# Optimization experiments

Hardware: AMD Instinct MI355X
Metric: run time of the kernel (lower is better)

Reference implementation:

```python
import jax, jax.numpy as jnp
import numpy as np

DIM = 768
HEADS = 12
HEAD_DIM = DIM // HEADS
WS = 32                      # window_size (Wh == Ww)
N = WS * WS + 1              # tokens = patches + CLS
B = 8
NUM_REL = (2 * WS - 1) * (2 * WS - 1) + 3


def _rel_pos_index():
    # Mirrors the torch buffer construction (meshgrid indexing='ij').
    coords = np.stack(np.meshgrid(np.arange(WS), np.arange(WS), indexing='ij')).reshape(2, -1)
    rel = (coords[:, :, None] - coords[:, None, :]).transpose(1, 2, 0)  # [M, M, 2]
    rel[..., 0] += WS - 1
    rel[..., 1] += WS - 1
    rel[..., 0] *= 2 * WS - 1
    idx = np.zeros((N, N), dtype=np.int32)
    idx[1:, 1:] = rel.sum(-1)
    idx[0, :] = NUM_REL - 3
    idx[:, 0] = NUM_REL - 2
    idx[0, 0] = NUM_REL - 1
    return idx


def setup_inputs() -> dict:
    key = jax.random.key(0)
    ks = jax.random.split(key, 4)
    s = DIM ** -0.5
    return {
        "x": jax.random.normal(ks[0], (B, N, DIM), dtype=jnp.float32),
        "qkv_w": jax.random.normal(ks[1], (3 * DIM, DIM), dtype=jnp.float32) * s,
        "q_bias": jnp.zeros((DIM,), dtype=jnp.float32),
        "v_bias": jnp.zeros((DIM,), dtype=jnp.float32),
        "rpb_table": jax.random.normal(ks[2], (NUM_REL, HEADS), dtype=jnp.float32) * 0.02,
        "proj_w": jax.random.normal(ks[3], (DIM, DIM), dtype=jnp.float32) * s,
        "proj_b": jnp.zeros((DIM,), dtype=jnp.float32),
        "rel_pos_index": jnp.asarray(_rel_pos_index()),
    }


def reference(x, qkv_w, q_bias, v_bias, rpb_table, proj_w, proj_b, rel_pos_index):
    Bx, Nx, C = x.shape
    scale = HEAD_DIM ** -0.5
    # qkv bias = [q_bias, zeros, v_bias] (k has no bias)
    qkv_bias = jnp.concatenate([q_bias, jnp.zeros_like(v_bias), v_bias])
    qkv = x @ qkv_w.T + qkv_bias                           # [B, N, 3*C]
    qkv = qkv.reshape(Bx, Nx, 3, HEADS, HEAD_DIM).transpose(2, 0, 3, 1, 4)
    q, k, v = qkv[0] * scale, qkv[1], qkv[2]               # [B, H, N, d]
    attn = jnp.einsum('bhqd,bhkd->bhqk', q, k)             # [B, H, N, N]
    rpb = rpb_table[rel_pos_index]                         # [N, N, H] gather
    attn = attn + rpb.transpose(2, 0, 1)[None]             # broadcast over batch
    attn = jax.nn.softmax(attn, axis=-1)
    out = jnp.einsum('bhqk,bhkd->bhqd', attn, v)           # [B, H, N, d]
    out = out.transpose(0, 2, 1, 3).reshape(Bx, Nx, -1)    # [B, N, C]
    return out @ proj_w.T + proj_b
```

## Files before the change

kernel.cpp:

```cpp
#include <hip/hip_runtime.h>

typedef _Float16 f16;
typedef __attribute__((ext_vector_type(8))) _Float16 f16x8;
typedef __attribute__((ext_vector_type(4))) float f32x4;

#define BATCH 8
#define NTOK 1025
#define DIM 768
#define HEADS 12
#define HD 64
#define MTOT (BATCH * NTOK)
#define MPAD 8320
#define NQP 1088
#define NKP 1088
#define KTILES 17
#define NUMREL 3972

__device__ __forceinline__ int imin(int a, int b) { return a < b ? a : b; }

__device__ __forceinline__ void gl_lds16(const f16* g, f16* l) {
  __builtin_amdgcn_global_load_lds(
      (const __attribute__((address_space(1))) unsigned int*)g,
      (__attribute__((address_space(3))) unsigned int*)l, 16, 0, 0);
}

__global__ __launch_bounds__(256) void cast3(const float* __restrict__ s0,
                                             f16* __restrict__ d0, int n0,
                                             const float* __restrict__ s1,
                                             f16* __restrict__ d1, int n1,
                                             const float* __restrict__ s2,
                                             f16* __restrict__ d2, int n2) {
  const float* s = (blockIdx.y == 0) ? s0 : (blockIdx.y == 1) ? s1 : s2;
  f16* d = (blockIdx.y == 0) ? d0 : (blockIdx.y == 1) ? d1 : d2;
  int n = (blockIdx.y == 0) ? n0 : (blockIdx.y == 1) ? n1 : n2;
  for (size_t i = ((size_t)blockIdx.x * 256 + threadIdx.x) * 8; i < (size_t)n;
       i += (size_t)gridDim.x * 256 * 8) {
    float4 a = *(const float4*)(s + i);
    float4 b = *(const float4*)(s + i + 4);
    f16x8 r;
    r[0] = (f16)a.x; r[1] = (f16)a.y; r[2] = (f16)a.z; r[3] = (f16)a.w;
    r[4] = (f16)b.x; r[5] = (f16)b.y; r[6] = (f16)b.z; r[7] = (f16)b.w;
    *(f16x8*)(d + i) = r;
  }
}

__device__ __forceinline__ float rpb_bias(const float* __restrict__ rpb, int qg,
                                          int kg, int h) {
  int idx;
  if (kg == 0) {
    idx = (qg == 0) ? (NUMREL - 1) : (NUMREL - 2);
  } else if (qg == 0) {
    idx = NUMREL - 3;
  } else {
    int qq = imin(qg, 1024) - 1, kk = imin(kg, 1024) - 1;
    int di = (qq >> 5) - (kk >> 5);
    int dj = (qq & 31) - (kk & 31);
    idx = (di + 31) * 63 + (dj + 31);
  }
  return rpb[idx * HEADS + h];
}

__global__ __launch_bounds__(256) void bias_pre(const float* __restrict__ rpb,
                                                f16* __restrict__ bias_sw) {
  const int tile = blockIdx.x;
  const int h = blockIdx.y;
  const int qt = tile / KTILES, kt = tile % KTILES;
  const int tid = threadIdx.x;
  const int lane = tid & 63, w = tid >> 6;
  const int lr = lane & 15, lg = lane >> 4;
  f16 vals[16];
#pragma unroll
  for (int c = 0; c < 4; c++) {
#pragma unroll
    for (int r = 0; r < 4; r++) {
      int qg = qt * 64 + w * 16 + lg * 4 + r;
      int kg = kt * 64 + c * 16 + lr;
      float v = (kg >= NTOK) ? -30000.f : rpb_bias(rpb, qg, kg, h);
      vals[c * 4 + r] = (f16)v;
    }
  }
  size_t off = ((((size_t)h * KTILES + qt) * KTILES + kt) * 256 + tid) * 16;
  *(f16x8*)(bias_sw + off) = *(const f16x8*)(&vals[0]);
  *(f16x8*)(bias_sw + off + 8) = *(const f16x8*)(&vals[8]);
}

__global__ __launch_bounds__(256) void qkv_gemm(
    const f16* __restrict__ Ah, const f16* __restrict__ Bh,
    const float* __restrict__ q_bias, const float* __restrict__ v_bias,
    f16* __restrict__ qb, f16* __restrict__ kb, f16* __restrict__ vtb) {
  __shared__ f16 As[128][64];
  __shared__ f16 Bs[128][64];
  const int tid = threadIdx.x;
  const int lane = tid & 63, w = tid >> 6;
  const int wm = w >> 1, wn = w & 1;
  const int lr = lane & 15, lg = lane >> 4;
  const int tM = blockIdx.x;
  const int tN = blockIdx.y;
  const int r8 = lane >> 3, ch = lane & 7;
  const int swch = ch ^ r8;
  const int lr7 = lr & 7;

  const f16* Abase = Ah + ((size_t)tM * 128 + r8) * DIM + swch * 8;
  const f16* Bbase = Bh + ((size_t)tN * 128 + r8) * DIM + swch * 8;

  f32x4 acc[4][4] = {};

  for (int kt = 0; kt < DIM; kt += 64) {
#pragma unroll
    for (int pp = 0; pp < 4; pp++) {
      int rowb = w * 32 + pp * 8;
      gl_lds16(Abase + (size_t)rowb * DIM + kt, &As[rowb][0]);
      gl_lds16(Bbase + (size_t)rowb * DIM + kt, &Bs[rowb][0]);
    }
    __syncthreads();
#pragma unroll
    for (int ks = 0; ks < 2; ks++) {
      f16x8 af[4], bfr[4];
      int rc = ((ks * 4 + lg) ^ lr7) * 8;
#pragma unroll
      for (int i = 0; i < 4; i++) {
        af[i] = *(const f16x8*)(&As[wm * 64 + i * 16 + lr][rc]);
        bfr[i] = *(const f16x8*)(&Bs[wn * 64 + i * 16 + lr][rc]);
      }
#pragma unroll
      for (int mi = 0; mi < 4; mi++)
#pragma unroll
        for (int ni = 0; ni < 4; ni++)
          acc[mi][ni] = __builtin_amdgcn_mfma_f32_16x16x32_f16(
              af[mi], bfr[ni], acc[mi][ni], 0, 0, 0);
    }
    __syncthreads();
  }

  const int which = tN / 6;
  const int nb = tN % 6;
#pragma unroll
  for (int mi = 0; mi < 4; mi++) {
#pragma unroll
    for (int ni = 0; ni < 4; ni++) {
      int ncol = nb * 128 + wn * 64 + ni * 16 + lr;
      int h = ncol >> 6, dd = ncol & 63;
      float bias = 0.f;
      if (which == 0) bias = q_bias[ncol];
      if (which == 2) bias = v_bias[ncol];
#pragma unroll
      for (int r = 0; r < 4; r++) {
        int m = tM * 128 + wm * 64 + mi * 16 + lg * 4 + r;
        if (m >= MTOT) continue;
        int b = m / NTOK;
        int t = m - b * NTOK;
        int bh = b * HEADS + h;
        float v = acc[mi][ni][r] + bias;
        if (which == 0)
          qb[((size_t)bh * NQP + t) * HD + dd] = (f16)(v * 0.125f);
        else if (which == 1)
          kb[((size_t)bh * NKP + t) * HD + dd] = (f16)v;
        else
          vtb[((size_t)bh * HD + dd) * NKP + t] = (f16)v;
      }
    }
  }
}

__global__ __launch_bounds__(256) void attn_kernel(
    const f16* __restrict__ qb, const f16* __restrict__ kb,
    const f16* __restrict__ vtb, const f16* __restrict__ bias_sw,
    f16* __restrict__ ob) {
  __shared__ f16 Ks[2][64][64];
  __shared__ f16 Vs[2][64][64];
  __shared__ f16 Plds[4][16][72];
  const int tid = threadIdx.x;
  const int lane = tid & 63, w = tid >> 6;
  const int lr = lane & 15, lg = lane >> 4;
  const int bidx = blockIdx.x;
  const int qt = bidx % KTILES;
  const int bh = bidx / KTILES;
  const int h = bh % HEADS;
  const int b = bh / HEADS;
  const int q0 = qt * 64 + w * 16;

  const f16* kbase = kb + (size_t)bh * NKP * HD;
  const f16* vbase = vtb + (size_t)bh * HD * NKP;
  const f16* bptr =
      bias_sw + (((size_t)(h * KTILES + qt) * KTILES) * 256 + tid) * 16;

  const int srow8 = lane >> 3;
  const int sch = lane & 7;
  const int swch = sch ^ srow8;

#pragma unroll
  for (int pp = 0; pp < 2; pp++) {
    int p = w * 2 + pp;
    int row = p * 8 + srow8;
    gl_lds16(kbase + (size_t)row * HD + swch * 8, &Ks[0][p * 8][0]);
    gl_lds16(vbase + (size_t)row * NKP + swch * 8, &Vs[0][p * 8][0]);
  }

  const f16* qptr = qb + ((size_t)bh * NQP + q0 + lr) * HD + lg * 8;
  f16x8 aq0 = *(const f16x8*)(qptr);
  f16x8 aq1 = *(const f16x8*)(qptr + 32);

  f16x8 bb0 = *(const f16x8*)(bptr);
  f16x8 bb1 = *(const f16x8*)(bptr + 8);

  float lsum[4] = {0.f, 0.f, 0.f, 0.f};
  f32x4 oacc[4] = {};
  const int sw8 = lr & 7;

  for (int kt = 0; kt < KTILES; kt++) {
    const int bi = kt & 1;
    __syncthreads();
    if (kt + 1 < KTILES) {
#pragma unroll
      for (int pp = 0; pp < 2; pp++) {
        int p = w * 2 + pp;
        int row = p * 8 + srow8;
        gl_lds16(kbase + (size_t)((kt + 1) * 64 + row) * HD + swch * 8,
                 &Ks[bi ^ 1][p * 8][0]);
        gl_lds16(vbase + (size_t)row * NKP + (kt + 1) * 64 + swch * 8,
                 &Vs[bi ^ 1][p * 8][0]);
      }
    }
    f16x8 nb0 = {}, nb1 = {};
    if (kt + 1 < KTILES) {
      nb0 = *(const f16x8*)(bptr + (size_t)(kt + 1) * 4096);
      nb1 = *(const f16x8*)(bptr + (size_t)(kt + 1) * 4096 + 8);
    }
    f32x4 s[4];
#pragma unroll
    for (int c = 0; c < 4; c++) {
      const f16* src = (c < 2) ? (const f16*)&bb0 : (const f16*)&bb1;
#pragma unroll
      for (int r = 0; r < 4; r++) s[c][r] = (float)src[(c & 1) * 4 + r];
    }
#pragma unroll
    for (int c = 0; c < 4; c++) {
      f16x8 bk0 = *(const f16x8*)(&Ks[bi][c * 16 + lr][(lg ^ sw8) * 8]);
      f16x8 bk1 = *(const f16x8*)(&Ks[bi][c * 16 + lr][((lg + 4) ^ sw8) * 8]);
      s[c] = __builtin_amdgcn_mfma_f32_16x16x32_f16(aq0, bk0, s[c], 0, 0, 0);
      s[c] = __builtin_amdgcn_mfma_f32_16x16x32_f16(aq1, bk1, s[c], 0, 0, 0);
    }
#pragma unroll
    for (int c = 0; c < 4; c++)
#pragma unroll
      for (int r = 0; r < 4; r++) {
        float p = __expf(s[c][r]);
        s[c][r] = p;
        lsum[r] += p;
      }
#pragma unroll
    for (int c = 0; c < 4; c++)
#pragma unroll
      for (int r = 0; r < 4; r++)
        Plds[w][lg * 4 + r][c * 16 + lr] = (f16)s[c][r];
    f16x8 ap0 = *(const f16x8*)(&Plds[w][lr][lg * 8]);
    f16x8 ap1 = *(const f16x8*)(&Plds[w][lr][32 + lg * 8]);
#pragma unroll
    for (int dblk = 0; dblk < 4; dblk++) {
      f16x8 bv0 = *(const f16x8*)(&Vs[bi][dblk * 16 + lr][(lg ^ sw8) * 8]);
      f16x8 bv1 = *(const f16x8*)(&Vs[bi][dblk * 16 + lr][((lg + 4) ^ sw8) * 8]);
      oacc[dblk] =
          __builtin_amdgcn_mfma_f32_16x16x32_f16(ap0, bv0, oacc[dblk], 0, 0, 0);
      oacc[dblk] =
          __builtin_amdgcn_mfma_f32_16x16x32_f16(ap1, bv1, oacc[dblk], 0, 0, 0);
    }
    bb0 = nb0;
    bb1 = nb1;
  }
  float ltot[4];
#pragma unroll
  for (int r = 0; r < 4; r++) {
    float ls = lsum[r];
    ls += __shfl_xor(ls, 1);
    ls += __shfl_xor(ls, 2);
    ls += __shfl_xor(ls, 4);
    ls += __shfl_xor(ls, 8);
    ltot[r] = ls;
  }
#pragma unroll
  for (int dblk = 0; dblk < 4; dblk++) {
#pragma unroll
    for (int r = 0; r < 4; r++) {
      int qg = q0 + lg * 4 + r;
      if (qg >= NTOK) continue;
      float v = oacc[dblk][r] / ltot[r];
      ob[((size_t)(b * NTOK + qg)) * DIM + h * HD + dblk * 16 + lr] = (f16)v;
    }
  }
}

__global__ __launch_bounds__(256) void proj_gemm(const f16* __restrict__ Ah,
                                                 const f16* __restrict__ Bh,
                                                 const float* __restrict__ pb,
                                                 float* __restrict__ out) {
  __shared__ f16 As[128][64];
  __shared__ f16 Bs[64][64];
  const int tid = threadIdx.x;
  const int lane = tid & 63, w = tid >> 6;
  const int wm = w >> 1, wn = w & 1;
  const int lr = lane & 15, lg = lane >> 4;
  const int tM = blockIdx.x;
  const int tN = blockIdx.y;
  const int r8 = lane >> 3, ch = lane & 7;
  const int swch = ch ^ r8;
  const int lr7 = lr & 7;

  const f16* Abase = Ah + ((size_t)tM * 128 + r8) * DIM + swch * 8;
  const f16* Bbase = Bh + ((size_t)tN * 64 + r8) * DIM + swch * 8;

  f32x4 acc[4][2] = {};

  for (int kt = 0; kt < DIM; kt += 64) {
#pragma unroll
    for (int pp = 0; pp < 4; pp++) {
      int rowb = w * 32 + pp * 8;
      gl_lds16(Abase + (size_t)rowb * DIM + kt, &As[rowb][0]);
    }
#pragma unroll
    for (int pp = 0; pp < 2; pp++) {
      int rowb = w * 16 + pp * 8;
      gl_lds16(Bbase + (size_t)rowb * DIM + kt, &Bs[rowb][0]);
    }
    __syncthreads();
#pragma unroll
    for (int ks = 0; ks < 2; ks++) {
      f16x8 af[4], bfr[2];
      int rc = ((ks * 4 + lg) ^ lr7) * 8;
#pragma unroll
      for (int i = 0; i < 4; i++)
        af[i] = *(const f16x8*)(&As[wm * 64 + i * 16 + lr][rc]);
#pragma unroll
      for (int i = 0; i < 2; i++)
        bfr[i] = *(const f16x8*)(&Bs[wn * 32 + i * 16 + lr][rc]);
#pragma unroll
      for (int mi = 0; mi < 4; mi++)
#pragma unroll
        for (int ni = 0; ni < 2; ni++)
          acc[mi][ni] = __builtin_amdgcn_mfma_f32_16x16x32_f16(
              af[mi], bfr[ni], acc[mi][ni], 0, 0, 0);
    }
    __syncthreads();
  }

#pragma unroll
  for (int mi = 0; mi < 4; mi++) {
#pragma unroll
    for (int ni = 0; ni < 2; ni++) {
      int n = tN * 64 + wn * 32 + ni * 16 + lr;
      float bias = pb[n];
#pragma unroll
      for (int r = 0; r < 4; r++) {
        int m = tM * 128 + wm * 64 + mi * 16 + lg * 4 + r;
        if (m >= MTOT) continue;
        out[(size_t)m * DIM + n] = acc[mi][ni][r] + bias;
      }
    }
  }
}

extern "C" void kernel_launch(void* const* d_in, const int* in_sizes, int n_in,
                              void* d_out, int out_size, void* d_ws,
                              size_t ws_size, hipStream_t stream) {
  const float* x = (const float*)d_in[0];
  const float* qkv_w = (const float*)d_in[1];
  const float* q_bias = (const float*)d_in[2];
  const float* v_bias = (const float*)d_in[3];
  const float* rpb = (const float*)d_in[4];
  const float* proj_w = (const float*)d_in[5];
  const float* proj_b = (const float*)d_in[6];
  float* out = (float*)d_out;

  f16* xh = (f16*)d_ws;
  f16* wh = xh + (size_t)MPAD * DIM;
  f16* pwh = wh + (size_t)3 * DIM * DIM;
  f16* qb = pwh + (size_t)DIM * DIM;
  size_t qsz = (size_t)BATCH * HEADS * NQP * HD;
  f16* kb = qb + qsz;
  f16* vtb = kb + qsz;
  f16* ob = vtb + qsz;
  f16* bias_sw = ob + (size_t)MPAD * DIM;

  cast3<<<dim3(1024, 3), 256, 0, stream>>>(
      x, xh, MTOT * DIM, qkv_w, wh, 3 * DIM * DIM, proj_w, pwh, DIM * DIM);
  bias_pre<<<dim3(KTILES * KTILES, HEADS), 256, 0, stream>>>(rpb, bias_sw);
  qkv_gemm<<<dim3(65, 18), 256, 0, stream>>>(xh, wh, q_bias, v_bias, qb, kb,
                                             vtb);
  attn_kernel<<<dim3(BATCH * HEADS * KTILES), 256, 0, stream>>>(qb, kb, vtb,
                                                                bias_sw, ob);
  proj_gemm<<<dim3(65, 12), 256, 0, stream>>>(ob, pwh, proj_b, out);
}
```

Measured before the change: 316.9 us.

## Double-buffer GEMM K-loops and widen attention query tile with transposed score layout

```diff
diff --git a/kernel.cpp b/kernel.cpp
--- a/kernel.cpp
+++ b/kernel.cpp
@@ -1,6 +1,7 @@
 #include <hip/hip_runtime.h>
 
 typedef _Float16 f16;
+typedef __attribute__((ext_vector_type(4))) _Float16 f16x4;
 typedef __attribute__((ext_vector_type(8))) _Float16 f16x8;
 typedef __attribute__((ext_vector_type(4))) float f32x4;
 
@@ -11,9 +12,8 @@
 #define HD 64
 #define MTOT (BATCH * NTOK)
 #define MPAD 8320
-#define NQP 1088
+#define NQP2 1152
 #define NKP 1088
-#define KTILES 17
 #define NUMREL 3972
 
 __device__ __forceinline__ int imin(int a, int b) { return a < b ? a : b; }
@@ -61,75 +61,80 @@
 }
 
 __global__ __launch_bounds__(256) void bias_pre(const float* __restrict__ rpb,
-                                                f16* __restrict__ bias_sw) {
-  const int tile = blockIdx.x;
+                                                f16* __restrict__ tbl) {
+  const int kt = blockIdx.x / 17;
+  const int qb17 = blockIdx.x % 17;
   const int h = blockIdx.y;
-  const int qt = tile / KTILES, kt = tile % KTILES;
   const int tid = threadIdx.x;
-  const int lane = tid & 63, w = tid >> 6;
-  const int lr = lane & 15, lg = lane >> 4;
+  const int q = qb17 * 64 + (tid >> 2);
+  const int lg = tid & 3;
   f16 vals[16];
 #pragma unroll
-  for (int c = 0; c < 4; c++) {
+  for (int c = 0; c < 4; c++)
 #pragma unroll
     for (int r = 0; r < 4; r++) {
-      int qg = qt * 64 + w * 16 + lg * 4 + r;
-      int kg = kt * 64 + c * 16 + lr;
-      float v = (kg >= NTOK) ? -30000.f : rpb_bias(rpb, qg, kg, h);
+      int kv = kt * 64 + c * 16 + lg * 4 + r;
+      float v = (kv >= NTOK) ? -30000.f : rpb_bias(rpb, q, kv, h);
       vals[c * 4 + r] = (f16)v;
     }
-  }
-  size_t off = ((((size_t)h * KTILES + qt) * KTILES + kt) * 256 + tid) * 16;
-  *(f16x8*)(bias_sw + off) = *(const f16x8*)(&vals[0]);
-  *(f16x8*)(bias_sw + off + 8) = *(const f16x8*)(&vals[8]);
+  size_t off = ((((size_t)h * 17 + kt) * NKP + q) * 4 + lg) * 16;
+  *(f16x8*)(tbl + off) = *(const f16x8*)(&vals[0]);
+  *(f16x8*)(tbl + off + 8) = *(const f16x8*)(&vals[8]);
 }
 
 __global__ __launch_bounds__(256) void qkv_gemm(
     const f16* __restrict__ Ah, const f16* __restrict__ Bh,
     const float* __restrict__ q_bias, const float* __restrict__ v_bias,
     f16* __restrict__ qb, f16* __restrict__ kb, f16* __restrict__ vtb) {
-  __shared__ f16 As[128][64];
-  __shared__ f16 Bs[128][64];
+  __shared__ f16 As[2][128][32];
+  __shared__ f16 Bs[2][128][32];
   const int tid = threadIdx.x;
   const int lane = tid & 63, w = tid >> 6;
   const int wm = w >> 1, wn = w & 1;
   const int lr = lane & 15, lg = lane >> 4;
   const int tM = blockIdx.x;
   const int tN = blockIdx.y;
-  const int r8 = lane >> 3, ch = lane & 7;
-  const int swch = ch ^ r8;
-  const int lr7 = lr & 7;
-
-  const f16* Abase = Ah + ((size_t)tM * 128 + r8) * DIM + swch * 8;
-  const f16* Bbase = Bh + ((size_t)tN * 128 + r8) * DIM + swch * 8;
+  const int rr = lane >> 2;
+  const int swc = (lane & 3) ^ (rr & 3);
+  const int lr3 = lr & 3;
+
+  const f16* Ab = Ah + ((size_t)tM * 128 + rr) * DIM + swc * 8;
+  const f16* Bb = Bh + ((size_t)tN * 128 + rr) * DIM + swc * 8;
+
+#pragma unroll
+  for (int pp = 0; pp < 2; pp++) {
+    int p = w * 2 + pp;
+    gl_lds16(Ab + (size_t)p * 16 * DIM, &As[0][p * 16][0]);
+    gl_lds16(Bb + (size_t)p * 16 * DIM, &Bs[0][p * 16][0]);
+  }
 
   f32x4 acc[4][4] = {};
 
-  for (int kt = 0; kt < DIM; kt += 64) {
-#pragma unroll
-    for (int pp = 0; pp < 4; pp++) {
-      int rowb = w * 32 + pp * 8;
-      gl_lds16(Abase + (size_t)rowb * DIM + kt, &As[rowb][0]);
-      gl_lds16(Bbase + (size_t)rowb * DIM + kt, &Bs[rowb][0]);
-    }
+  for (int kt = 0; kt < 24; kt++) {
+    const int bi = kt & 1;
     __syncthreads();
-#pragma unroll
-    for (int ks = 0; ks < 2; ks++) {
-      f16x8 af[4], bfr[4];
-      int rc = ((ks * 4 + lg) ^ lr7) * 8;
-#pragma unroll
-      for (int i = 0; i < 4; i++) {
-        af[i] = *(const f16x8*)(&As[wm * 64 + i * 16 + lr][rc]);
-        bfr[i] = *(const f16x8*)(&Bs[wn * 64 + i * 16 + lr][rc]);
-      }
-#pragma unroll
-      for (int mi = 0; mi < 4; mi++)
-#pragma unroll
-        for (int ni = 0; ni < 4; ni++)
-          acc[mi][ni] = __builtin_amdgcn_mfma_f32_16x16x32_f16(
-              af[mi], bfr[ni], acc[mi][ni], 0, 0, 0);
-    }
-    __syncthreads();
+    if (kt + 1 < 24) {
+#pragma unroll
+      for (int pp = 0; pp < 2; pp++) {
+        int p = w * 2 + pp;
+        gl_lds16(Ab + (size_t)p * 16 * DIM + (kt + 1) * 32,
+                 &As[bi ^ 1][p * 16][0]);
+        gl_lds16(Bb + (size_t)p * 16 * DIM + (kt + 1) * 32,
+                 &Bs[bi ^ 1][p * 16][0]);
+      }
+    }
+    f16x8 af[4], bf[4];
+#pragma unroll
+    for (int i = 0; i < 4; i++) {
+      af[i] = *(const f16x8*)(&As[bi][wm * 64 + i * 16 + lr][(lg ^ lr3) * 8]);
+      bf[i] = *(const f16x8*)(&Bs[bi][wn * 64 + i * 16 + lr][(lg ^ lr3) * 8]);
+    }
+#pragma unroll
+    for (int mi = 0; mi < 4; mi++)
+#pragma unroll
+      for (int ni = 0; ni < 4; ni++)
+        acc[mi][ni] = __builtin_amdgcn_mfma_f32_16x16x32_f16(
+            af[mi], bf[ni], acc[mi][ni], 0, 0, 0);
   }
 
   const int which = tN / 6;
@@ -152,7 +157,7 @@
         int bh = b * HEADS + h;
         float v = acc[mi][ni][r] + bias;
         if (which == 0)
-          qb[((size_t)bh * NQP + t) * HD + dd] = (f16)(v * 0.125f);
+          qb[((size_t)bh * NQP2 + t) * HD + dd] = (f16)(v * 0.125f);
         else if (which == 1)
           kb[((size_t)bh * NKP + t) * HD + dd] = (f16)v;
         else
@@ -164,7 +169,7 @@
 
 __global__ __launch_bounds__(256) void attn_kernel(
     const f16* __restrict__ qb, const f16* __restrict__ kb,
-    const f16* __restrict__ vtb, const f16* __restrict__ bias_sw,
+    const f16* __restrict__ vtb, const f16* __restrict__ tbl,
     f16* __restrict__ ob) {
   __shared__ f16 Ks[2][64][64];
   __shared__ f16 Vs[2][64][64];
@@ -172,21 +177,16 @@
   const int tid = threadIdx.x;
   const int lane = tid & 63, w = tid >> 6;
   const int lr = lane & 15, lg = lane >> 4;
-  const int bidx = blockIdx.x;
-  const int qt = bidx % KTILES;
-  const int bh = bidx / KTILES;
-  const int h = bh % HEADS;
-  const int b = bh / HEADS;
-  const int q0 = qt * 64 + w * 16;
+  const int qblk = blockIdx.x % 9;
+  const int bh = blockIdx.x / 9;
+  const int h = bh % HEADS, b = bh / HEADS;
+  const int q0 = qblk * 128 + w * 32;
 
   const f16* kbase = kb + (size_t)bh * NKP * HD;
   const f16* vbase = vtb + (size_t)bh * HD * NKP;
-  const f16* bptr =
-      bias_sw + (((size_t)(h * KTILES + qt) * KTILES) * 256 + tid) * 16;
 
   const int srow8 = lane >> 3;
-  const int sch = lane & 7;
-  const int swch = sch ^ srow8;
+  const int swch = (lane & 7) ^ srow8;
 
 #pragma unroll
   for (int pp = 0; pp < 2; pp++) {
@@ -196,21 +196,36 @@
     gl_lds16(vbase + (size_t)row * NKP + swch * 8, &Vs[0][p * 8][0]);
   }
 
-  const f16* qptr = qb + ((size_t)bh * NQP + q0 + lr) * HD + lg * 8;
-  f16x8 aq0 = *(const f16x8*)(qptr);
-  f16x8 aq1 = *(const f16x8*)(qptr + 32);
-
-  f16x8 bb0 = *(const f16x8*)(bptr);
-  f16x8 bb1 = *(const f16x8*)(bptr + 8);
-
-  float lsum[4] = {0.f, 0.f, 0.f, 0.f};
-  f32x4 oacc[4] = {};
+  f16x8 aq[2][2];
+#pragma unroll
+  for (int g = 0; g < 2; g++) {
+    const f16* qp = qb + ((size_t)bh * NQP2 + q0 + g * 16 + lr) * HD + lg * 8;
+    aq[g][0] = *(const f16x8*)(qp);
+    aq[g][1] = *(const f16x8*)(qp + 32);
+  }
+
+  const f16* bp[2];
+#pragma unroll
+  for (int g = 0; g < 2; g++) {
+    int qt = imin(q0 + g * 16 + lr, NKP - 1);
+    bp[g] = tbl + (((size_t)h * 17 * NKP + qt) * 4 + lg) * 16;
+  }
+  f16x8 bb[2][2];
+#pragma unroll
+  for (int g = 0; g < 2; g++) {
+    bb[g][0] = *(const f16x8*)(bp[g]);
+    bb[g][1] = *(const f16x8*)(bp[g] + 8);
+  }
+
+  float lsum[2] = {0.f, 0.f};
+  f32x4 oacc[2][4] = {};
   const int sw8 = lr & 7;
-
-  for (int kt = 0; kt < KTILES; kt++) {
+  const size_t ktstride = (size_t)NKP * 64;
+
+  for (int kt = 0; kt < 17; kt++) {
     const int bi = kt & 1;
     __syncthreads();
-    if (kt + 1 < KTILES) {
+    if (kt + 1 < 17) {
 #pragma unroll
       for (int pp = 0; pp < 2; pp++) {
         int p = w * 2 + pp;
@@ -221,71 +236,90 @@
                  &Vs[bi ^ 1][p * 8][0]);
       }
     }
-    f16x8 nb0 = {}, nb1 = {};
-    if (kt + 1 < KTILES) {
-      nb0 = *(const f16x8*)(bptr + (size_t)(kt + 1) * 4096);
-      nb1 = *(const f16x8*)(bptr + (size_t)(kt + 1) * 4096 + 8);
-    }
-    f32x4 s[4];
+    f16x8 nb[2][2] = {};
+    if (kt + 1 < 17) {
+#pragma unroll
+      for (int g = 0; g < 2; g++) {
+        const f16* p8 = bp[g] + (size_t)(kt + 1) * ktstride;
+        nb[g][0] = *(const f16x8*)(p8);
+        nb[g][1] = *(const f16x8*)(p8 + 8);
+      }
+    }
+    f32x4 s[2][4];
+#pragma unroll
+    for (int g = 0; g < 2; g++)
+#pragma unroll
+      for (int c = 0; c < 4; c++) {
+        const f16* src = (const f16*)&bb[g][c >> 1];
+#pragma unroll
+        for (int r = 0; r < 4; r++) s[g][c][r] = (float)src[(c & 1) * 4 + r];
+      }
 #pragma unroll
     for (int c = 0; c < 4; c++) {
-      const f16* src = (c < 2) ? (const f16*)&bb0 : (const f16*)&bb1;
-#pragma unroll
-      for (int r = 0; r < 4; r++) s[c][r] = (float)src[(c & 1) * 4 + r];
-    }
-#pragma unroll
-    for (int c = 0; c < 4; c++) {
-      f16x8 bk0 = *(const f16x8*)(&Ks[bi][c * 16 + lr][(lg ^ sw8) * 8]);
-      f16x8 bk1 = *(const f16x8*)(&Ks[bi][c * 16 + lr][((lg + 4) ^ sw8) * 8]);
-      s[c] = __builtin_amdgcn_mfma_f32_16x16x32_f16(aq0, bk0, s[c], 0, 0, 0);
-      s[c] = __builtin_amdgcn_mfma_f32_16x16x32_f16(aq1, bk1, s[c], 0, 0, 0);
-    }
-#pragma unroll
-    for (int c = 0; c < 4; c++)
+      f16x8 kf0 = *(const f16x8*)(&Ks[bi][c * 16 + lr][(lg ^ sw8) * 8]);
+      f16x8 kf1 = *(const f16x8*)(&Ks[bi][c * 16 + lr][((lg + 4) ^ sw8) * 8]);
+      s[0][c] = __builtin_amdgcn_mfma_f32_16x16x32_f16(kf0, aq[0][0], s[0][c], 0, 0, 0);
+      s[0][c] = __builtin_amdgcn_mfma_f32_16x16x32_f16(kf1, aq[0][1], s[0][c], 0, 0, 0);
+      s[1][c] = __builtin_amdgcn_mfma_f32_16x16x32_f16(kf0, aq[1][0], s[1][c], 0, 0, 0);
+      s[1][c] = __builtin_amdgcn_mfma_f32_16x16x32_f16(kf1, aq[1][1], s[1][c], 0, 0, 0);
+    }
+#pragma unroll
+    for (int g = 0; g < 2; g++)
+#pragma unroll
+      for (int c = 0; c < 4; c++)
+#pragma unroll
+        for (int r = 0; r < 4; r++) {
+          float p = __expf(s[g][c][r]);
+          s[g][c][r] = p;
+          lsum[g] += p;
+        }
+    f16x8 ap[2][2];
+#pragma unroll
+    for (int g = 0; g < 2; g++) {
+#pragma unroll
+      for (int c = 0; c < 4; c++) {
+        f16x4 pk;
+        pk[0] = (f16)s[g][c][0];
+        pk[1] = (f16)s[g][c][1];
+        pk[2] = (f16)s[g][c][2];
+        pk[3] = (f16)s[g][c][3];
+        *(f16x4*)(&Plds[w][lr][c * 16 + lg * 4]) = pk;
+      }
+      ap[g][0] = *(const f16x8*)(&Plds[w][lr][lg * 8]);
+      ap[g][1] = *(const f16x8*)(&Plds[w][lr][32 + lg * 8]);
+    }
+#pragma unroll
+    for (int dblk = 0; dblk < 4; dblk++) {
+      f16x8 vf0 = *(const f16x8*)(&Vs[bi][dblk * 16 + lr][(lg ^ sw8) * 8]);
+      f16x8 vf1 = *(const f16x8*)(&Vs[bi][dblk * 16 + lr][((lg + 4) ^ sw8) * 8]);
+      oacc[0][dblk] = __builtin_amdgcn_mfma_f32_16x16x32_f16(ap[0][0], vf0, oacc[0][dblk], 0, 0, 0);
+      oacc[0][dblk] = __builtin_amdgcn_mfma_f32_16x16x32_f16(ap[0][1], vf1, oacc[0][dblk], 0, 0, 0);
+      oacc[1][dblk] = __builtin_amdgcn_mfma_f32_16x16x32_f16(ap[1][0], vf0, oacc[1][dblk], 0, 0, 0);
+      oacc[1][dblk] = __builtin_amdgcn_mfma_f32_16x16x32_f16(ap[1][1], vf1, oacc[1][dblk], 0, 0, 0);
+    }
+#pragma unroll
+    for (int g = 0; g < 2; g++) {
+      bb[g][0] = nb[g][0];
+      bb[g][1] = nb[g][1];
+    }
+  }
+#pragma unroll
+  for (int g = 0; g < 2; g++) {
+    float ls = lsum[g];
+    ls += __shfl_xor(ls, 16);
+    ls += __shfl_xor(ls, 32);
+    float inv[4];
+#pragma unroll
+    for (int r = 0; r < 4; r++) inv[r] = 1.f / __shfl(ls, lg * 4 + r);
+#pragma unroll
+    for (int dblk = 0; dblk < 4; dblk++)
 #pragma unroll
       for (int r = 0; r < 4; r++) {
-        float p = __expf(s[c][r]);
-        s[c][r] = p;
-        lsum[r] += p;
-      }
-#pragma unroll
-    for (int c = 0; c < 4; c++)
-#pragma unroll
-      for (int r = 0; r < 4; r++)
-        Plds[w][lg * 4 + r][c * 16 + lr] = (f16)s[c][r];
-    f16x8 ap0 = *(const f16x8*)(&Plds[w][lr][lg * 8]);
-    f16x8 ap1 = *(const f16x8*)(&Plds[w][lr][32 + lg * 8]);
-#pragma unroll
-    for (int dblk = 0; dblk < 4; dblk++) {
-      f16x8 bv0 = *(const f16x8*)(&Vs[bi][dblk * 16 + lr][(lg ^ sw8) * 8]);
-      f16x8 bv1 = *(const f16x8*)(&Vs[bi][dblk * 16 + lr][((lg + 4) ^ sw8) * 8]);
-      oacc[dblk] =
-          __builtin_amdgcn_mfma_f32_16x16x32_f16(ap0, bv0, oacc[dblk], 0, 0, 0);
-      oacc[dblk] =
-          __builtin_amdgcn_mfma_f32_16x16x32_f16(ap1, bv1, oacc[dblk], 0, 0, 0);
-    }
-    bb0 = nb0;
-    bb1 = nb1;
-  }
-  float ltot[4];
-#pragma unroll
-  for (int r = 0; r < 4; r++) {
-    float ls = lsum[r];
-    ls += __shfl_xor(ls, 1);
-    ls += __shfl_xor(ls, 2);
-    ls += __shfl_xor(ls, 4);
-    ls += __shfl_xor(ls, 8);
-    ltot[r] = ls;
-  }
-#pragma unroll
-  for (int dblk = 0; dblk < 4; dblk++) {
-#pragma unroll
-    for (int r = 0; r < 4; r++) {
-      int qg = q0 + lg * 4 + r;
-      if (qg >= NTOK) continue;
-      float v = oacc[dblk][r] / ltot[r];
-      ob[((size_t)(b * NTOK + qg)) * DIM + h * HD + dblk * 16 + lr] = (f16)v;
-    }
+        int qg = q0 + g * 16 + lg * 4 + r;
+        if (qg >= NTOK) continue;
+        float v = oacc[g][dblk][r] * inv[r];
+        ob[((size_t)(b * NTOK + qg)) * DIM + h * HD + dblk * 16 + lr] = (f16)v;
+      }
   }
 }
 
@@ -293,53 +327,55 @@
                                                  const f16* __restrict__ Bh,
                                                  const float* __restrict__ pb,
                                                  float* __restrict__ out) {
-  __shared__ f16 As[128][64];
-  __shared__ f16 Bs[64][64];
+  __shared__ f16 As[2][128][32];
+  __shared__ f16 Bs[2][64][32];
   const int tid = threadIdx.x;
   const int lane = tid & 63, w = tid >> 6;
   const int wm = w >> 1, wn = w & 1;
   const int lr = lane & 15, lg = lane >> 4;
   const int tM = blockIdx.x;
   const int tN = blockIdx.y;
-  const int r8 = lane >> 3, ch = lane & 7;
-  const int swch = ch ^ r8;
-  const int lr7 = lr & 7;
-
-  const f16* Abase = Ah + ((size_t)tM * 128 + r8) * DIM + swch * 8;
-  const f16* Bbase = Bh + ((size_t)tN * 64 + r8) * DIM + swch * 8;
+  const int rr = lane >> 2;
+  const int swc = (lane & 3) ^ (rr & 3);
+  const int lr3 = lr & 3;
+
+  const f16* Ab = Ah + ((size_t)tM * 128 + rr) * DIM + swc * 8;
+  const f16* Bb = Bh + ((size_t)tN * 64 + rr) * DIM + swc * 8;
+
+#pragma unroll
+  for (int pp = 0; pp < 2; pp++) {
+    int p = w * 2 + pp;
+    gl_lds16(Ab + (size_t)p * 16 * DIM, &As[0][p * 16][0]);
+  }
+  gl_lds16(Bb + (size_t)w * 16 * DIM, &Bs[0][w * 16][0]);
 
   f32x4 acc[4][2] = {};
 
-  for (int kt = 0; kt < DIM; kt += 64) {
-#pragma unroll
-    for (int pp = 0; pp < 4; pp++) {
-      int rowb = w * 32 + pp * 8;
-      gl_lds16(Abase + (size_t)rowb * DIM + kt, &As[rowb][0]);
-    }
-#pragma unroll
-    for (int pp = 0; pp < 2; pp++) {
-      int rowb = w * 16 + pp * 8;
-      gl_lds16(Bbase + (size_t)rowb * DIM + kt, &Bs[rowb][0]);
-    }
+  for (int kt = 0; kt < 24; kt++) {
+    const int bi = kt & 1;
     __syncthreads();
-#pragma unroll
-    for (int ks = 0; ks < 2; ks++) {
-      f16x8 af[4], bfr[2];
-      int rc = ((ks * 4 + lg) ^ lr7) * 8;
-#pragma unroll
-      for (int i = 0; i < 4; i++)
-        af[i] = *(const f16x8*)(&As[wm * 64 + i * 16 + lr][rc]);
-#pragma unroll
-      for (int i = 0; i < 2; i++)
-        bfr[i] = *(const f16x8*)(&Bs[wn * 32 + i * 16 + lr][rc]);
-#pragma unroll
-      for (int mi = 0; mi < 4; mi++)
-#pragma unroll
-        for (int ni = 0; ni < 2; ni++)
-          acc[mi][ni] = __builtin_amdgcn_mfma_f32_16x16x32_f16(
-              af[mi], bfr[ni], acc[mi][ni], 0, 0, 0);
-    }
-    __syncthreads();
+    if (kt + 1 < 24) {
+#pragma unroll
+      for (int pp = 0; pp < 2; pp++) {
+        int p = w * 2 + pp;
+        gl_lds16(Ab + (size_t)p * 16 * DIM + (kt + 1) * 32,
+                 &As[bi ^ 1][p * 16][0]);
+      }
+      gl_lds16(Bb + (size_t)w * 16 * DIM + (kt + 1) * 32, &Bs[bi ^ 1][w * 16][0]);
+    }
+    f16x8 af[4], bf[2];
+#pragma unroll
+    for (int i = 0; i < 4; i++)
+      af[i] = *(const f16x8*)(&As[bi][wm * 64 + i * 16 + lr][(lg ^ lr3) * 8]);
+#pragma unroll
+    for (int i = 0; i < 2; i++)
+      bf[i] = *(const f16x8*)(&Bs[bi][wn * 32 + i * 16 + lr][(lg ^ lr3) * 8]);
+#pragma unroll
+    for (int mi = 0; mi < 4; mi++)
+#pragma unroll
+      for (int ni = 0; ni < 2; ni++)
+        acc[mi][ni] = __builtin_amdgcn_mfma_f32_16x16x32_f16(
+            af[mi], bf[ni], acc[mi][ni], 0, 0, 0);
   }
 
 #pragma unroll
@@ -374,18 +410,17 @@
   f16* wh = xh + (size_t)MPAD * DIM;
   f16* pwh = wh + (size_t)3 * DIM * DIM;
   f16* qb = pwh + (size_t)DIM * DIM;
-  size_t qsz = (size_t)BATCH * HEADS * NQP * HD;
-  f16* kb = qb + qsz;
-  f16* vtb = kb + qsz;
-  f16* ob = vtb + qsz;
-  f16* bias_sw = ob + (size_t)MPAD * DIM;
+  f16* kb = qb + (size_t)BATCH * HEADS * NQP2 * HD;
+  f16* vtb = kb + (size_t)BATCH * HEADS * NKP * HD;
+  f16* ob = vtb + (size_t)BATCH * HEADS * NKP * HD;
+  f16* tbl = ob + (size_t)MPAD * DIM;
 
   cast3<<<dim3(1024, 3), 256, 0, stream>>>(
       x, xh, MTOT * DIM, qkv_w, wh, 3 * DIM * DIM, proj_w, pwh, DIM * DIM);
-  bias_pre<<<dim3(KTILES * KTILES, HEADS), 256, 0, stream>>>(rpb, bias_sw);
+  bias_pre<<<dim3(17 * 17, HEADS), 256, 0, stream>>>(rpb, tbl);
   qkv_gemm<<<dim3(65, 18), 256, 0, stream>>>(xh, wh, q_bias, v_bias, qb, kb,
                                              vtb);
-  attn_kernel<<<dim3(BATCH * HEADS * KTILES), 256, 0, stream>>>(qb, kb, vtb,
-                                                                bias_sw, ob);
+  attn_kernel<<<dim3(BATCH * HEADS * 9), 256, 0, stream>>>(qb, kb, vtb, tbl,
+                                                           ob);
   proj_gemm<<<dim3(65, 12), 256, 0, stream>>>(ob, pwh, proj_b, out);
 }
```

Result: faster. 297.4 us (-6.2%).
